# Optimization experiments

Hardware: AMD Instinct MI355X
Metric: run time of the kernel (lower is better)

Reference implementation:

```python
import jax, jax.numpy as jnp
import numpy as np

IN_F = 256
OUT_F = 64
LRELU_SLOPE = 0.2


def setup_inputs() -> dict:
    key = jax.random.key(0)
    k1, k2, k3 = jax.random.split(key, 3)
    B, N = 4, 4096
    h = jax.random.normal(k1, (B, N, IN_F), dtype=jnp.float32)
    # xavier_uniform with gain=1.414
    def xavier(k, shape, gain=1.414):
        fan_in, fan_out = shape[0], shape[1]
        bound = gain * np.sqrt(6.0 / (fan_in + fan_out))
        return jax.random.uniform(k, shape, jnp.float32, -bound, bound)
    W = xavier(k2, (IN_F, OUT_F))
    a = xavier(k3, (2 * OUT_F, 1))
    return {"h": h, "W": W, "a": a}


def reference(h, W, a):
    # Wh: (B, N, F_out)
    Wh = jnp.matmul(h, W)
    # Algebraic split of a = [a1; a2]: score(i,j) = Wh_i @ a1 + Wh_j @ a2
    a1 = a[:OUT_F, 0]   # (F,)
    a2 = a[OUT_F:, 0]   # (F,)
    e1 = Wh @ a1        # (B, N)
    e2 = Wh @ a2        # (B, N)
    e = e1[:, :, None] + e2[:, None, :]   # (B, N, N)
    return jnp.where(e > 0, e, LRELU_SLOPE * e)
```

## Files before the change

### kernel.cpp

```cpp
#include <hip/hip_runtime.h>
#include <hip/hip_bf16.h>


#define B_DIM 4
#define N_DIM 4096
#define IN_F 256
#define OUT_F 64
#define SLOPE 0.2f

typedef float f32x4 __attribute__((ext_vector_type(4)));

__global__ void gat_dots(const float* __restrict__ h, const float* __restrict__ W,
                         const float* __restrict__ a,
                         float* __restrict__ e1, float* __restrict__ e2) {
    __shared__ float v1s[IN_F];
    __shared__ float v2s[IN_F];
    const int t = threadIdx.x;

    {
        float s1 = 0.f, s2 = 0.f;
        const float* wr = W + t * OUT_F;
        #pragma unroll 8
        for (int j = 0; j < OUT_F; ++j) {
            float w = wr[j];
            s1 += w * a[j];
            s2 += w * a[OUT_F + j];
        }
        v1s[t] = s1;
        v2s[t] = s2;
    }
    __syncthreads();

    const int lane = t & 63;
    const int wid  = t >> 6;
    const f32x4 v1 = reinterpret_cast<const f32x4*>(v1s)[lane];
    const f32x4 v2 = reinterpret_cast<const f32x4*>(v2s)[lane];
    const int base = blockIdx.x * 64 + wid * 16;

    for (int r = 0; r < 16; ++r) {
        const int row = base + r;
        const f32x4 hv = reinterpret_cast<const f32x4*>(h + (size_t)row * IN_F)[lane];
        float d1 = hv.x * v1.x + hv.y * v1.y + hv.z * v1.z + hv.w * v1.w;
        float d2 = hv.x * v2.x + hv.y * v2.y + hv.z * v2.z + hv.w * v2.w;
        #pragma unroll
        for (int m = 32; m >= 1; m >>= 1) {
            d1 += __shfl_xor(d1, m);
            d2 += __shfl_xor(d2, m);
        }
        if (lane == 0) {
            e1[row] = d1;
            e2[row] = d2;
        }
    }
}

__global__ void gat_epilogue(const float* __restrict__ e1, const float* __restrict__ e2,
                             float* __restrict__ out) {
    const int row = blockIdx.x;
    const int b   = row >> 12;
    const float s = e1[row];
    const f32x4* e2v = reinterpret_cast<const f32x4*>(e2 + b * N_DIM);
    f32x4* outv = reinterpret_cast<f32x4*>(out + (size_t)row * N_DIM);

    #pragma unroll
    for (int k = 0; k < 4; ++k) {
        const int c = threadIdx.x + k * 256;
        const f32x4 t = e2v[c];
        f32x4 o;
        float ex = s + t.x; o.x = fmaxf(ex, SLOPE * ex);
        float ey = s + t.y; o.y = fmaxf(ey, SLOPE * ey);
        float ez = s + t.z; o.z = fmaxf(ez, SLOPE * ez);
        float ew = s + t.w; o.w = fmaxf(ew, SLOPE * ew);
        __builtin_nontemporal_store(o, &outv[c]);
    }
}

extern "C" void kernel_launch(void* const* d_in, const int* in_sizes, int n_in,
                              void* d_out, int out_size, void* d_ws, size_t ws_size,
                              hipStream_t stream) {
    const float* h = (const float*)d_in[0];
    const float* W = (const float*)d_in[1];
    const float* a = (const float*)d_in[2];

    float* ws = (float*)d_ws;
    float* e1 = ws;
    float* e2 = ws + 16384;

    gat_dots<<<256, 256, 0, stream>>>(h, W, a, e1, e2);
    gat_epilogue<<<B_DIM * N_DIM, 256, 0, stream>>>(e1, e2, (float*)d_out);
}
```

Before: 62.26 us.

## Reuse e2 registers across 8 rows per block and widen dots grid

The epilogue now has each block handle 8 output rows, loading the e2 row segment into registers once and reusing it for all 8 rows instead of reloading per row. Stores switch from nontemporal to regular stores. The dot-product kernel processes 4 rows per wave instead of 16 and launches 4x more blocks for more parallelism on h loading. The change trades fewer blocks in the epilogue for register reuse, and regular stores may pollute cache on the 256MB output write.

```diff
diff --git a/kernel.cpp b/kernel.cpp
--- a/kernel.cpp
+++ b/kernel.cpp
@@ -35,9 +35,10 @@
     const int wid  = t >> 6;
     const f32x4 v1 = reinterpret_cast<const f32x4*>(v1s)[lane];
     const f32x4 v2 = reinterpret_cast<const f32x4*>(v2s)[lane];
-    const int base = blockIdx.x * 64 + wid * 16;
+    const int base = blockIdx.x * 16 + wid * 4;
 
-    for (int r = 0; r < 16; ++r) {
+    #pragma unroll
+    for (int r = 0; r < 4; ++r) {
         const int row = base + r;
         const f32x4 hv = reinterpret_cast<const f32x4*>(h + (size_t)row * IN_F)[lane];
         float d1 = hv.x * v1.x + hv.y * v1.y + hv.z * v1.z + hv.w * v1.w;
@@ -56,22 +57,32 @@
 
 __global__ void gat_epilogue(const float* __restrict__ e1, const float* __restrict__ e2,
                              float* __restrict__ out) {
-    const int row = blockIdx.x;
-    const int b   = row >> 12;
-    const float s = e1[row];
+    const int rowBase = blockIdx.x * 8;
+    const int b       = rowBase >> 12;
+    const int tid     = threadIdx.x;
+
     const f32x4* e2v = reinterpret_cast<const f32x4*>(e2 + b * N_DIM);
-    f32x4* outv = reinterpret_cast<f32x4*>(out + (size_t)row * N_DIM);
+    const f32x4 c0 = e2v[tid];
+    const f32x4 c1 = e2v[tid + 256];
+    const f32x4 c2 = e2v[tid + 512];
+    const f32x4 c3 = e2v[tid + 768];
 
-    #pragma unroll
-    for (int k = 0; k < 4; ++k) {
-        const int c = threadIdx.x + k * 256;
-        const f32x4 t = e2v[c];
-        f32x4 o;
-        float ex = s + t.x; o.x = fmaxf(ex, SLOPE * ex);
-        float ey = s + t.y; o.y = fmaxf(ey, SLOPE * ey);
-        float ez = s + t.z; o.z = fmaxf(ez, SLOPE * ez);
-        float ew = s + t.w; o.w = fmaxf(ew, SLOPE * ew);
-        __builtin_nontemporal_store(o, &outv[c]);
+    for (int r = 0; r < 8; ++r) {
+        const int row = rowBase + r;
+        const float s = e1[row];
+        f32x4* outv = reinterpret_cast<f32x4*>(out + (size_t)row * N_DIM);
+        f32x4 o0, o1, o2, o3;
+        #define LRELU(dst, src) { \
+            float ex = s + (src).x; (dst).x = fmaxf(ex, SLOPE * ex); \
+            float ey = s + (src).y; (dst).y = fmaxf(ey, SLOPE * ey); \
+            float ez = s + (src).z; (dst).z = fmaxf(ez, SLOPE * ez); \
+            float ew = s + (src).w; (dst).w = fmaxf(ew, SLOPE * ew); }
+        LRELU(o0, c0) LRELU(o1, c1) LRELU(o2, c2) LRELU(o3, c3)
+        #undef LRELU
+        outv[tid]       = o0;
+        outv[tid + 256] = o1;
+        outv[tid + 512] = o2;
+        outv[tid + 768] = o3;
     }
 }
 
@@ -86,6 +97,6 @@
     float* e1 = ws;
     float* e2 = ws + 16384;
 
-    gat_dots<<<256, 256, 0, stream>>>(h, W, a, e1, e2);
-    gat_epilogue<<<B_DIM * N_DIM, 256, 0, stream>>>(e1, e2, (float*)d_out);
+    gat_dots<<<1024, 256, 0, stream>>>(h, W, a, e1, e2);
+    gat_epilogue<<<2048, 256, 0, stream>>>(e1, e2, (float*)d_out);
 }
```

Result: faster. 60.39 us (-3.0%).
